# Kernel optimization log

Hardware: AMD Instinct MI355X
Metric: run time of the kernel (lower is better)

The kernel has to match this reference:

```python
import jax, jax.numpy as jnp
import numpy as np

H = 1024       # hidden_size
VOCAB = 32000  # output_size
L = 128        # max_length
B = 64         # batch


def setup_inputs() -> dict:
    key = jax.random.key(0)
    ks = jax.random.split(key, 16)
    inp = {
        "input_ids": jax.random.randint(ks[0], (1, B), 0, VOCAB),
        "hidden": jax.random.normal(ks[1], (1, B, H), jnp.float32),
        "encoder_outputs": jax.random.normal(ks[2], (L, B, H), jnp.float32),
        # parameters
        "emb": jax.random.normal(ks[3], (VOCAB, H), jnp.float32) * 0.02,
        "attn_W": jax.random.normal(ks[4], (H, 2 * H), jnp.float32) * 0.02,
        "attn_b": jnp.zeros((H,), jnp.float32),
        "v": jax.random.uniform(ks[5], (H,), jnp.float32),
        "w_ih": jax.random.normal(ks[6], (3 * H, 2 * H), jnp.float32) * 0.02,
        "w_hh": jax.random.normal(ks[7], (3 * H, H), jnp.float32) * 0.02,
        "b_ih": jnp.zeros((3 * H,), jnp.float32),
        "b_hh": jnp.zeros((3 * H,), jnp.float32),
        "out_W": jax.random.normal(ks[8], (VOCAB, 3 * H), jnp.float32) * 0.02,
        "out_b": jnp.zeros((VOCAB,), jnp.float32),
    }
    return inp


def reference(input_ids, hidden, encoder_outputs, emb, attn_W, attn_b, v,
              w_ih, w_hh, b_ih, b_hh, out_W, out_b):
    # Dropout in eval mode (identity).
    embedded = emb[input_ids]                      # [1, B, H]
    eo = jnp.transpose(encoder_outputs, (1, 0, 2))  # [B, L, H]
    h0 = hidden[0]                                  # [B, H]

    # Additive (Bahdanau) attention score
    h_rep = jnp.broadcast_to(h0[:, None, :], (eo.shape[0], eo.shape[1], h0.shape[-1]))
    cat = jnp.concatenate([eo, h_rep], axis=-1)     # [B, L, 2H]
    energy = jnp.tanh(jnp.einsum('blk,hk->blh', cat, attn_W) + attn_b)  # [B, L, H]
    scores = jnp.einsum('blh,h->bl', energy, v)     # [B, L]
    attention = jax.nn.softmax(scores, axis=-1)     # [B, L]
    weighted = jnp.einsum('bl,blh->bh', attention, eo)  # [B, H]

    # GRU cell (single layer, single timestep), PyTorch gate order r,z,n
    x = jnp.concatenate([embedded[0], weighted], axis=-1)  # [B, 2H]
    gx = x @ w_ih.T + b_ih                                  # [B, 3H]
    gh = h0 @ w_hh.T + b_hh                                 # [B, 3H]
    xr, xz, xn = jnp.split(gx, 3, axis=-1)
    hr, hz, hn = jnp.split(gh, 3, axis=-1)
    r = jax.nn.sigmoid(xr + hr)
    z = jax.nn.sigmoid(xz + hz)
    n = jnp.tanh(xn + r * hn)
    h_new = (1.0 - z) * n + z * h0                          # [B, H]

    out_cat = jnp.concatenate([h_new, weighted, embedded[0]], axis=-1)  # [B, 3H]
    output = out_cat @ out_W.T + out_b                      # [B, VOCAB]
    return output, h_new[None], attention[:, None, :]
```

## Files before the change

### kernel.cpp

```cpp
#include <hip/hip_runtime.h>
#include <math.h>

#define Hdim 1024
#define VOC 32000
#define LSEQ 128
#define BSZ 64

typedef __attribute__((ext_vector_type(8))) short bf16x8;
typedef __attribute__((ext_vector_type(4))) float f32x4;

__device__ __forceinline__ float fast_tanhf(float x) {
    return 1.0f - 2.0f / (__expf(2.0f * x) + 1.0f);
}
__device__ __forceinline__ float sigmoidf(float x) {
    return 1.0f / (1.0f + __expf(-x));
}
__device__ __forceinline__ short f2bf(float f) {
    unsigned u = __float_as_uint(f);
    unsigned r = (u + 0x7fffu + ((u >> 16) & 1u)) >> 16;
    return (short)r;
}

__device__ __forceinline__ void stage16(const float* __restrict__ src, short* dst) {
    f32x4 v0 = *(const f32x4*)(src);
    f32x4 v1 = *(const f32x4*)(src + 4);
    f32x4 v2 = *(const f32x4*)(src + 8);
    f32x4 v3 = *(const f32x4*)(src + 12);
    bf16x8 p0, p1;
    p0[0] = f2bf(v0[0]); p0[1] = f2bf(v0[1]); p0[2] = f2bf(v0[2]); p0[3] = f2bf(v0[3]);
    p0[4] = f2bf(v1[0]); p0[5] = f2bf(v1[1]); p0[6] = f2bf(v1[2]); p0[7] = f2bf(v1[3]);
    p1[0] = f2bf(v2[0]); p1[1] = f2bf(v2[1]); p1[2] = f2bf(v2[2]); p1[3] = f2bf(v2[3]);
    p1[4] = f2bf(v3[0]); p1[5] = f2bf(v3[1]); p1[6] = f2bf(v3[2]); p1[7] = f2bf(v3[3]);
    *(bf16x8*)(dst) = p0;
    *(bf16x8*)(dst + 8) = p1;
}

__global__ __launch_bounds__(256) void convert_bf16(
    const float* __restrict__ enc, const float* __restrict__ attnW,
    const float* __restrict__ hidden,
    short* __restrict__ enc_bf, short* __restrict__ attnW_bf,
    short* __restrict__ hidden_bf)
{
    const int NG_ENC = (LSEQ * BSZ * Hdim) / 8;
    const int NG_AW  = (Hdim * 2 * Hdim) / 8;
    const int NG_H   = (BSZ * Hdim) / 8;
    const int total = NG_ENC + NG_AW + NG_H;
    for (int g = blockIdx.x * 256 + threadIdx.x; g < total; g += gridDim.x * 256) {
        const float* src; short* dst; int idx;
        if (g < NG_ENC)              { src = enc;    dst = enc_bf;    idx = g; }
        else if (g < NG_ENC + NG_AW) { src = attnW;  dst = attnW_bf;  idx = g - NG_ENC; }
        else                         { src = hidden; dst = hidden_bf; idx = g - NG_ENC - NG_AW; }
        f32x4 a = *(const f32x4*)(src + (size_t)idx * 8);
        f32x4 b = *(const f32x4*)(src + (size_t)idx * 8 + 4);
        bf16x8 p;
        p[0] = f2bf(a[0]); p[1] = f2bf(a[1]); p[2] = f2bf(a[2]); p[3] = f2bf(a[3]);
        p[4] = f2bf(b[0]); p[5] = f2bf(b[1]); p[6] = f2bf(b[2]); p[7] = f2bf(b[3]);
        *(bf16x8*)(dst + (size_t)idx * 8) = p;
    }
}

__global__ __launch_bounds__(256) void ugemm(
    const short* __restrict__ A,
    const short* __restrict__ B,
    float* __restrict__ C)
{
    __shared__ short As[64 * 72];
    __shared__ short Bs[128 * 72];

    const int t = threadIdx.x;
    const int lane = t & 63, wave = t >> 6;
    const int lr = lane & 15, kh = lane >> 4;
    const int n0 = blockIdx.x * 128;
    const int kstart = blockIdx.y * 256;
    float* Cp = C + (size_t)blockIdx.y * (BSZ * Hdim);

    const int ar = t >> 2, ac = (t & 3) * 16;
    const int br = t >> 1, bc = (t & 1) * 32;

    f32x4 acc[4][2] = {};

    for (int k0 = 0; k0 < 256; k0 += 64) {
        const int kg = kstart + k0;
        {
            const short* s = A + (size_t)ar * Hdim + kg + ac;
            *(bf16x8*)(As + ar * 72 + ac)     = *(const bf16x8*)(s);
            *(bf16x8*)(As + ar * 72 + ac + 8) = *(const bf16x8*)(s + 8);
        }
        {
            const short* s = B + (size_t)(n0 + br) * (2 * Hdim) + kg + bc;
            short* d = Bs + br * 72 + bc;
            *(bf16x8*)(d)      = *(const bf16x8*)(s);
            *(bf16x8*)(d + 8)  = *(const bf16x8*)(s + 8);
            *(bf16x8*)(d + 16) = *(const bf16x8*)(s + 16);
            *(bf16x8*)(d + 24) = *(const bf16x8*)(s + 24);
        }
        __syncthreads();
#pragma unroll
        for (int kk = 0; kk < 64; kk += 32) {
            bf16x8 af[4], bfr[2];
#pragma unroll
            for (int mi = 0; mi < 4; ++mi)
                af[mi] = *(const bf16x8*)(As + (mi * 16 + lr) * 72 + kk + kh * 8);
#pragma unroll
            for (int ni = 0; ni < 2; ++ni)
                bfr[ni] = *(const bf16x8*)(Bs + (wave * 32 + ni * 16 + lr) * 72 + kk + kh * 8);
#pragma unroll
            for (int mi = 0; mi < 4; ++mi)
#pragma unroll
                for (int ni = 0; ni < 2; ++ni)
                    acc[mi][ni] = __builtin_amdgcn_mfma_f32_16x16x32_bf16(
                        af[mi], bfr[ni], acc[mi][ni], 0, 0, 0);
        }
        __syncthreads();
    }

#pragma unroll
    for (int mi = 0; mi < 4; ++mi)
#pragma unroll
        for (int ni = 0; ni < 2; ++ni) {
            const int col = n0 + wave * 32 + ni * 16 + lr;
#pragma unroll
            for (int r = 0; r < 4; ++r) {
                const int row = mi * 16 + kh * 4 + r;
                Cp[(size_t)row * Hdim + col] = acc[mi][ni][r];
            }
        }
}

__global__ __launch_bounds__(512) void attn_scores_mfma(
    const short* __restrict__ enc_bf,
    const short* __restrict__ W1_bf,
    const float* __restrict__ u4,
    const float* __restrict__ attnb,
    const float* __restrict__ vvec,
    float* __restrict__ scores_part)
{
    __shared__ short As[128 * 72];
    __shared__ short Bs[128 * 72];
    __shared__ float red[8][64];
    __shared__ float u_lds[64 * 128];

    const int t = threadIdx.x;
    const int lane = t & 63, wave = t >> 6;
    const int wr = wave >> 2, wc = wave & 3;
    const int lr = lane & 15, kh = lane >> 4;
    const int m0 = blockIdx.x * 128;
    const int n0 = blockIdx.y * 128;

    const int srow = t >> 2, scol = (t & 3) * 16;

    for (int i = t; i < 64 * 128; i += 512) {
        const int b = i >> 7, hl = i & 127;
        const size_t g = (size_t)b * Hdim + n0 + hl;
        u_lds[i] = u4[g] + u4[65536 + g] + u4[2 * 65536 + g] + u4[3 * 65536 + g]
                 + attnb[n0 + hl];
    }

    f32x4 acc[4][2] = {};

    for (int kg = 0; kg < Hdim; kg += 64) {
        {
            const short* s = enc_bf + (size_t)(m0 + srow) * Hdim + kg + scol;
            *(bf16x8*)(As + srow * 72 + scol)     = *(const bf16x8*)(s);
            *(bf16x8*)(As + srow * 72 + scol + 8) = *(const bf16x8*)(s + 8);
        }
        {
            const short* s = W1_bf + (size_t)(n0 + srow) * (2 * Hdim) + kg + scol;
            *(bf16x8*)(Bs + srow * 72 + scol)     = *(const bf16x8*)(s);
            *(bf16x8*)(Bs + srow * 72 + scol + 8) = *(const bf16x8*)(s + 8);
        }
        __syncthreads();
#pragma unroll
        for (int kk = 0; kk < 64; kk += 32) {
            bf16x8 af[4], bfr[2];
#pragma unroll
            for (int mi = 0; mi < 4; ++mi)
                af[mi] = *(const bf16x8*)(As + (wr * 64 + mi * 16 + lr) * 72 + kk + kh * 8);
#pragma unroll
            for (int ni = 0; ni < 2; ++ni)
                bfr[ni] = *(const bf16x8*)(Bs + (wc * 32 + ni * 16 + lr) * 72 + kk + kh * 8);
#pragma unroll
            for (int mi = 0; mi < 4; ++mi)
#pragma unroll
                for (int ni = 0; ni < 2; ++ni)
                    acc[mi][ni] = __builtin_amdgcn_mfma_f32_16x16x32_bf16(
                        af[mi], bfr[ni], acc[mi][ni], 0, 0, 0);
        }
        __syncthreads();
    }

    float sv[16];
#pragma unroll
    for (int mi = 0; mi < 4; ++mi)
#pragma unroll
        for (int r = 0; r < 4; ++r) {
            const int lrow = mi * 16 + kh * 4 + r;
            const int b = lrow;
            float s = 0.0f;
#pragma unroll
            for (int ni = 0; ni < 2; ++ni) {
                const int hl = wc * 32 + ni * 16 + lr;
                const float e = fast_tanhf(acc[mi][ni][r] + u_lds[b * 128 + hl]);
                s += e * vvec[n0 + hl];
            }
            sv[mi * 4 + r] = s;
        }
#pragma unroll
    for (int i = 0; i < 16; ++i) {
#pragma unroll
        for (int d = 1; d < 16; d <<= 1)
            sv[i] += __shfl_xor(sv[i], d, 64);
    }
    if (lr == 0) {
#pragma unroll
        for (int mi = 0; mi < 4; ++mi)
#pragma unroll
            for (int r = 0; r < 4; ++r)
                red[wave][mi * 16 + kh * 4 + r] = sv[mi * 4 + r];
    }
    __syncthreads();
    if (t < 128) {
        const int wrr = t >> 6, lrow = t & 63;
        scores_part[(size_t)blockIdx.y * (LSEQ * BSZ) + m0 + t] =
            red[wrr * 4 + 0][lrow] + red[wrr * 4 + 1][lrow] +
            red[wrr * 4 + 2][lrow] + red[wrr * 4 + 3][lrow];
    }
}

__global__ __launch_bounds__(256) void softmax_weighted(
    const float* __restrict__ sp,
    const short* __restrict__ enc_bf,
    const int* __restrict__ ids,
    const float* __restrict__ emb,
    float* __restrict__ attn_out,
    short* __restrict__ x_bf,
    short* __restrict__ oc_bf)
{
    const int b = blockIdx.x, t = threadIdx.x;
    __shared__ float aw[LSEQ];
    __shared__ float red[128];

    {
        const int id = ids[b];
#pragma unroll
        for (int i = 0; i < 4; ++i) {
            const int h = t * 4 + i;
            const short e = f2bf(emb[(size_t)id * Hdim + h]);
            x_bf[(size_t)b * 2048 + h] = e;
            oc_bf[(size_t)b * 3072 + 2048 + h] = e;
        }
    }

    float s = 0.0f;
    if (t < 128) {
#pragma unroll
        for (int g = 0; g < 8; ++g) s += sp[g * (LSEQ * BSZ) + t * 64 + b];
        red[t] = s;
    }
    __syncthreads();
    for (int off = 64; off > 0; off >>= 1) {
        if (t < off) red[t] = fmaxf(red[t], red[t + off]);
        __syncthreads();
    }
    const float mx = red[0];
    __syncthreads();
    float e = 0.0f;
    if (t < 128) { e = __expf(s - mx); red[t] = e; }
    __syncthreads();
    for (int off = 64; off > 0; off >>= 1) {
        if (t < off) red[t] += red[t + off];
        __syncthreads();
    }
    const float inv = 1.0f / red[0];
    if (t < 128) {
        const float p = e * inv;
        aw[t] = p;
        attn_out[(size_t)b * LSEQ + t] = p;
    }
    __syncthreads();

#pragma unroll
    for (int c = 0; c < 2; ++c) {
        const int h = c * 512 + t * 2;
        float a0 = 0.0f, a1 = 0.0f;
        for (int l = 0; l < LSEQ; ++l) {
            const unsigned w = *(const unsigned*)(enc_bf + ((size_t)l * BSZ + b) * Hdim + h);
            const float p = aw[l];
            a0 = fmaf(p, __uint_as_float(w << 16), a0);
            a1 = fmaf(p, __uint_as_float(w & 0xffff0000u), a1);
        }
        const unsigned packed = (unsigned)(unsigned short)f2bf(a0)
                              | ((unsigned)(unsigned short)f2bf(a1) << 16);
        *(unsigned*)(x_bf + (size_t)b * 2048 + 1024 + h) = packed;
        *(unsigned*)(oc_bf + (size_t)b * 3072 + 1024 + h) = packed;
    }
}

__global__ __launch_bounds__(256) void gxgh_gemm(
    const short* __restrict__ x_bf, const float* __restrict__ w_ih,
    const short* __restrict__ hidden_bf, const float* __restrict__ w_hh,
    float* __restrict__ gx4, float* __restrict__ gh4)
{
    __shared__ short As[64 * 72];
    __shared__ short Bs[128 * 72];

    const int t = threadIdx.x;
    const int lane = t & 63, wave = t >> 6;
    const int lr = lane & 15, kh = lane >> 4;

    const short* A; const float* B; float* C; int lda, klen, n0;
    if (blockIdx.x < 24) {
        A = x_bf; B = w_ih; C = gx4; lda = 2048; klen = 512; n0 = blockIdx.x * 128;
    } else {
        A = hidden_bf; B = w_hh; C = gh4; lda = 1024; klen = 256; n0 = (blockIdx.x - 24) * 128;
    }
    const int kstart = blockIdx.y * klen;
    float* Cp = C + (size_t)blockIdx.y * (BSZ * 3 * Hdim);

    const int ar = t >> 2, ac = (t & 3) * 16;
    const int br = t >> 1, bc = (t & 1) * 32;

    f32x4 acc[4][2] = {};

    for (int k0 = 0; k0 < klen; k0 += 64) {
        const int kg = kstart + k0;
        {
            const short* s = A + (size_t)ar * lda + kg + ac;
            *(bf16x8*)(As + ar * 72 + ac)     = *(const bf16x8*)(s);
            *(bf16x8*)(As + ar * 72 + ac + 8) = *(const bf16x8*)(s + 8);
        }
        {
            const float* s = B + (size_t)(n0 + br) * lda + kg + bc;
            stage16(s,      Bs + br * 72 + bc);
            stage16(s + 16, Bs + br * 72 + bc + 16);
        }
        __syncthreads();
#pragma unroll
        for (int kk = 0; kk < 64; kk += 32) {
            bf16x8 af[4], bfr[2];
#pragma unroll
            for (int mi = 0; mi < 4; ++mi)
                af[mi] = *(const bf16x8*)(As + (mi * 16 + lr) * 72 + kk + kh * 8);
#pragma unroll
            for (int ni = 0; ni < 2; ++ni)
                bfr[ni] = *(const bf16x8*)(Bs + (wave * 32 + ni * 16 + lr) * 72 + kk + kh * 8);
#pragma unroll
            for (int mi = 0; mi < 4; ++mi)
#pragma unroll
                for (int ni = 0; ni < 2; ++ni)
                    acc[mi][ni] = __builtin_amdgcn_mfma_f32_16x16x32_bf16(
                        af[mi], bfr[ni], acc[mi][ni], 0, 0, 0);
        }
        __syncthreads();
    }

#pragma unroll
    for (int mi = 0; mi < 4; ++mi)
#pragma unroll
        for (int ni = 0; ni < 2; ++ni) {
            const int col = n0 + wave * 32 + ni * 16 + lr;
#pragma unroll
            for (int r = 0; r < 4; ++r) {
                const int row = mi * 16 + kh * 4 + r;
                Cp[(size_t)row * (3 * Hdim) + col] = acc[mi][ni][r];
            }
        }
}

__global__ __launch_bounds__(256) void gru_kernel(
    const float* __restrict__ gx4, const float* __restrict__ gh4,
    const float* __restrict__ b_ih, const float* __restrict__ b_hh,
    const float* __restrict__ h0,
    float* __restrict__ hnew_out, short* __restrict__ oc_bf)
{
    const int idx = blockIdx.x * 256 + threadIdx.x;
    const int b = idx >> 10, h = idx & 1023;
    const size_t g3 = (size_t)b * (3 * Hdim);
    const size_t P = (size_t)BSZ * 3 * Hdim;
    float xr = b_ih[h], xz = b_ih[Hdim + h], xn = b_ih[2 * Hdim + h];
    float hr = b_hh[h], hz = b_hh[Hdim + h], hn = b_hh[2 * Hdim + h];
#pragma unroll
    for (int s = 0; s < 4; ++s) {
        xr += gx4[s * P + g3 + h];
        xz += gx4[s * P + g3 + Hdim + h];
        xn += gx4[s * P + g3 + 2 * Hdim + h];
        hr += gh4[s * P + g3 + h];
        hz += gh4[s * P + g3 + Hdim + h];
        hn += gh4[s * P + g3 + 2 * Hdim + h];
    }
    const float r = sigmoidf(xr + hr);
    const float z = sigmoidf(xz + hz);
    const float n = fast_tanhf(xn + r * hn);
    const float hv = (1.0f - z) * n + z * h0[(size_t)b * Hdim + h];
    hnew_out[(size_t)b * Hdim + h] = hv;
    oc_bf[g3 + h] = f2bf(hv);
}

__global__ __launch_bounds__(256) void outproj_direct(
    const short* __restrict__ A,
    const float* __restrict__ B,
    const float* __restrict__ bias,
    float* __restrict__ logits)
{
    __shared__ short As[64 * 72];
    __shared__ short Bs[64 * 72];

    const int t = threadIdx.x;
    const int lane = t & 63, wave = t >> 6;
    const int lr = lane & 15, kh = lane >> 4;
    const int n0 = blockIdx.x * 64;
    const int sr = t >> 2, sc = (t & 3) * 16;

    f32x4 acc[4] = {};

    for (int kg = 0; kg < 3072; kg += 64) {
        {
            const short* s = A + (size_t)sr * 3072 + kg + sc;
            *(bf16x8*)(As + sr * 72 + sc)     = *(const bf16x8*)(s);
            *(bf16x8*)(As + sr * 72 + sc + 8) = *(const bf16x8*)(s + 8);
        }
        stage16(B + (size_t)(n0 + sr) * 3072 + kg + sc, Bs + sr * 72 + sc);
        __syncthreads();
#pragma unroll
        for (int kk = 0; kk < 64; kk += 32) {
            bf16x8 af[4], bfr;
#pragma unroll
            for (int mi = 0; mi < 4; ++mi)
                af[mi] = *(const bf16x8*)(As + (mi * 16 + lr) * 72 + kk + kh * 8);
            bfr = *(const bf16x8*)(Bs + (wave * 16 + lr) * 72 + kk + kh * 8);
#pragma unroll
            for (int mi = 0; mi < 4; ++mi)
                acc[mi] = __builtin_amdgcn_mfma_f32_16x16x32_bf16(af[mi], bfr, acc[mi], 0, 0, 0);
        }
        __syncthreads();
    }

    const int col = n0 + wave * 16 + lr;
    const float bb = bias[col];
#pragma unroll
    for (int mi = 0; mi < 4; ++mi)
#pragma unroll
        for (int r = 0; r < 4; ++r) {
            const int row = mi * 16 + kh * 4 + r;
            logits[(size_t)row * VOC + col] = acc[mi][r] + bb;
        }
}

extern "C" void kernel_launch(void* const* d_in, const int* in_sizes, int n_in,
                              void* d_out, int out_size, void* d_ws, size_t ws_size,
                              hipStream_t stream)
{
    const int*   ids    = (const int*)d_in[0];
    const float* hidden = (const float*)d_in[1];
    const float* enc    = (const float*)d_in[2];
    const float* emb    = (const float*)d_in[3];
    const float* attnW  = (const float*)d_in[4];
    const float* attnb  = (const float*)d_in[5];
    const float* vvec   = (const float*)d_in[6];
    const float* w_ih   = (const float*)d_in[7];
    const float* w_hh   = (const float*)d_in[8];
    const float* b_ih   = (const float*)d_in[9];
    const float* b_hh   = (const float*)d_in[10];
    const float* out_W  = (const float*)d_in[11];
    const float* out_b  = (const float*)d_in[12];

    float* out        = (float*)d_out;
    float* out_logits = out;
    float* out_hnew   = out + (size_t)BSZ * VOC;
    float* out_attn   = out_hnew + (size_t)BSZ * Hdim;

    float* ws = (float*)d_ws;
    short* enc_bf    = (short*)ws;
    short* attnW_bf  = (short*)(ws + 4194304);
    short* hidden_bf = (short*)(ws + 5242880);
    float* ws_u4  = ws + 5275648;
    float* ws_sp  = ws_u4 + 262144;
    short* x_bf   = (short*)(ws_sp + 65536);
    short* oc_bf  = (short*)(ws_sp + 131072);
    float* ws_gx4 = ws_sp + 229376;
    float* ws_gh4 = ws_gx4 + 786432;

    convert_bf16<<<dim3(1024), 256, 0, stream>>>(
        enc, attnW, hidden, enc_bf, attnW_bf, hidden_bf);

    ugemm<<<dim3(Hdim / 128, 4), 256, 0, stream>>>(
        hidden_bf, attnW_bf + Hdim, ws_u4);

    attn_scores_mfma<<<dim3(LSEQ / 2, 8), 512, 0, stream>>>(
        enc_bf, attnW_bf, ws_u4, attnb, vvec, ws_sp);

    softmax_weighted<<<dim3(BSZ), 256, 0, stream>>>(
        ws_sp, enc_bf, ids, emb, out_attn, x_bf, oc_bf);

    gxgh_gemm<<<dim3(48, 4), 256, 0, stream>>>(
        x_bf, w_ih, hidden_bf, w_hh, ws_gx4, ws_gh4);

    gru_kernel<<<dim3(BSZ * Hdim / 256), 256, 0, stream>>>(
        ws_gx4, ws_gh4, b_ih, b_hh, hidden, out_hnew, oc_bf);

    outproj_direct<<<dim3(VOC / 64), 256, 0, stream>>>(
        oc_bf, out_W, out_b, out_logits);
}
```

Baseline: 190.0 us.

## Stream weights directly into MFMA registers, drop LDS staging; split softmax-weighted over hidden

Replaces the LDS-staged GEMMs for the GRU gates and output projection with a shared streaming body. Each lane loads its fp32 weight row slice, converts it to bf16 in registers and feeds MFMA directly, with no shared memory or barriers. The activation A operand is read from global memory/L2 by each wave. The gate GEMM now uses 64-column tiles, doubling its grid. The softmax/weighted-sum kernel is split across 4 hidden-dimension groups with 128 threads each for more parallelism, and uses vectorised embedding loads. The trade is that A reads repeat across waves instead of being shared, in exchange for removing sync and LDS traffic in these memory-bound weight-streaming GEMMs.

```diff
diff --git a/kernel.cpp b/kernel.cpp
--- a/kernel.cpp
+++ b/kernel.cpp
@@ -19,20 +19,6 @@
     unsigned u = __float_as_uint(f);
     unsigned r = (u + 0x7fffu + ((u >> 16) & 1u)) >> 16;
     return (short)r;
-}
-
-__device__ __forceinline__ void stage16(const float* __restrict__ src, short* dst) {
-    f32x4 v0 = *(const f32x4*)(src);
-    f32x4 v1 = *(const f32x4*)(src + 4);
-    f32x4 v2 = *(const f32x4*)(src + 8);
-    f32x4 v3 = *(const f32x4*)(src + 12);
-    bf16x8 p0, p1;
-    p0[0] = f2bf(v0[0]); p0[1] = f2bf(v0[1]); p0[2] = f2bf(v0[2]); p0[3] = f2bf(v0[3]);
-    p0[4] = f2bf(v1[0]); p0[5] = f2bf(v1[1]); p0[6] = f2bf(v1[2]); p0[7] = f2bf(v1[3]);
-    p1[0] = f2bf(v2[0]); p1[1] = f2bf(v2[1]); p1[2] = f2bf(v2[2]); p1[3] = f2bf(v2[3]);
-    p1[4] = f2bf(v3[0]); p1[5] = f2bf(v3[1]); p1[6] = f2bf(v3[2]); p1[7] = f2bf(v3[3]);
-    *(bf16x8*)(dst) = p0;
-    *(bf16x8*)(dst + 8) = p1;
 }
 
 __global__ __launch_bounds__(256) void convert_bf16(
@@ -227,7 +213,7 @@
     }
 }
 
-__global__ __launch_bounds__(256) void softmax_weighted(
+__global__ __launch_bounds__(128) void softmax_weighted(
     const float* __restrict__ sp,
     const short* __restrict__ enc_bf,
     const int* __restrict__ ids,
@@ -236,27 +222,26 @@
     short* __restrict__ x_bf,
     short* __restrict__ oc_bf)
 {
-    const int b = blockIdx.x, t = threadIdx.x;
+    const int b = blockIdx.x, hg = blockIdx.y, t = threadIdx.x;
     __shared__ float aw[LSEQ];
-    __shared__ float red[128];
-
-    {
+    __shared__ float red[LSEQ];
+
+    if (hg == 0) {
         const int id = ids[b];
-#pragma unroll
-        for (int i = 0; i < 4; ++i) {
-            const int h = t * 4 + i;
-            const short e = f2bf(emb[(size_t)id * Hdim + h]);
-            x_bf[(size_t)b * 2048 + h] = e;
-            oc_bf[(size_t)b * 3072 + 2048 + h] = e;
-        }
+        const int h = t * 8;
+        f32x4 e0 = *(const f32x4*)(emb + (size_t)id * Hdim + h);
+        f32x4 e1 = *(const f32x4*)(emb + (size_t)id * Hdim + h + 4);
+        bf16x8 p;
+        p[0] = f2bf(e0[0]); p[1] = f2bf(e0[1]); p[2] = f2bf(e0[2]); p[3] = f2bf(e0[3]);
+        p[4] = f2bf(e1[0]); p[5] = f2bf(e1[1]); p[6] = f2bf(e1[2]); p[7] = f2bf(e1[3]);
+        *(bf16x8*)(x_bf + (size_t)b * 2048 + h) = p;
+        *(bf16x8*)(oc_bf + (size_t)b * 3072 + 2048 + h) = p;
     }
 
     float s = 0.0f;
-    if (t < 128) {
-#pragma unroll
-        for (int g = 0; g < 8; ++g) s += sp[g * (LSEQ * BSZ) + t * 64 + b];
-        red[t] = s;
-    }
+#pragma unroll
+    for (int g = 0; g < 8; ++g) s += sp[g * (LSEQ * BSZ) + t * 64 + b];
+    red[t] = s;
     __syncthreads();
     for (int off = 64; off > 0; off >>= 1) {
         if (t < off) red[t] = fmaxf(red[t], red[t + off]);
@@ -264,107 +249,94 @@
     }
     const float mx = red[0];
     __syncthreads();
-    float e = 0.0f;
-    if (t < 128) { e = __expf(s - mx); red[t] = e; }
+    const float e = __expf(s - mx);
+    red[t] = e;
     __syncthreads();
     for (int off = 64; off > 0; off >>= 1) {
         if (t < off) red[t] += red[t + off];
         __syncthreads();
     }
-    const float inv = 1.0f / red[0];
-    if (t < 128) {
-        const float p = e * inv;
-        aw[t] = p;
-        attn_out[(size_t)b * LSEQ + t] = p;
-    }
+    const float p = e / red[0];
+    aw[t] = p;
+    if (hg == 0) attn_out[(size_t)b * LSEQ + t] = p;
     __syncthreads();
 
-#pragma unroll
-    for (int c = 0; c < 2; ++c) {
-        const int h = c * 512 + t * 2;
-        float a0 = 0.0f, a1 = 0.0f;
-        for (int l = 0; l < LSEQ; ++l) {
-            const unsigned w = *(const unsigned*)(enc_bf + ((size_t)l * BSZ + b) * Hdim + h);
-            const float p = aw[l];
-            a0 = fmaf(p, __uint_as_float(w << 16), a0);
-            a1 = fmaf(p, __uint_as_float(w & 0xffff0000u), a1);
-        }
-        const unsigned packed = (unsigned)(unsigned short)f2bf(a0)
-                              | ((unsigned)(unsigned short)f2bf(a1) << 16);
-        *(unsigned*)(x_bf + (size_t)b * 2048 + 1024 + h) = packed;
-        *(unsigned*)(oc_bf + (size_t)b * 3072 + 1024 + h) = packed;
-    }
-}
-
-__global__ __launch_bounds__(256) void gxgh_gemm(
+    const int h = hg * 256 + t * 2;
+    float a0 = 0.0f, a1 = 0.0f;
+#pragma unroll 8
+    for (int l = 0; l < LSEQ; ++l) {
+        const unsigned w = *(const unsigned*)(enc_bf + ((size_t)l * BSZ + b) * Hdim + h);
+        const float pw = aw[l];
+        a0 = fmaf(pw, __uint_as_float(w << 16), a0);
+        a1 = fmaf(pw, __uint_as_float(w & 0xffff0000u), a1);
+    }
+    const unsigned packed = (unsigned)(unsigned short)f2bf(a0)
+                          | ((unsigned)(unsigned short)f2bf(a1) << 16);
+    *(unsigned*)(x_bf + (size_t)b * 2048 + 1024 + h) = packed;
+    *(unsigned*)(oc_bf + (size_t)b * 3072 + 1024 + h) = packed;
+}
+
+__device__ __forceinline__ void stream_body(
+    const short* __restrict__ A, int lda,
+    const float* __restrict__ B, int ldb,
+    const float* __restrict__ bias,
+    float* __restrict__ C, int ldc,
+    int n0, int kstart, int klen)
+{
+    const int t = threadIdx.x;
+    const int lane = t & 63, wave = t >> 6;
+    const int lr = lane & 15, kh = lane >> 4;
+
+    const float* Brow = B + (size_t)(n0 + wave * 16 + lr) * ldb + kh * 8 + kstart;
+    const short* Ab   = A + (size_t)lr * lda + kh * 8 + kstart;
+
+    f32x4 acc[4] = {};
+
+#pragma unroll 4
+    for (int kg = 0; kg < klen; kg += 32) {
+        f32x4 b0 = *(const f32x4*)(Brow + kg);
+        f32x4 b1 = *(const f32x4*)(Brow + kg + 4);
+        bf16x8 bfr;
+        bfr[0] = f2bf(b0[0]); bfr[1] = f2bf(b0[1]); bfr[2] = f2bf(b0[2]); bfr[3] = f2bf(b0[3]);
+        bfr[4] = f2bf(b1[0]); bfr[5] = f2bf(b1[1]); bfr[6] = f2bf(b1[2]); bfr[7] = f2bf(b1[3]);
+#pragma unroll
+        for (int mi = 0; mi < 4; ++mi) {
+            bf16x8 af = *(const bf16x8*)(Ab + (size_t)mi * 16 * lda + kg);
+            acc[mi] = __builtin_amdgcn_mfma_f32_16x16x32_bf16(af, bfr, acc[mi], 0, 0, 0);
+        }
+    }
+
+    const int col = n0 + wave * 16 + lr;
+    const float bb = bias ? bias[col] : 0.0f;
+#pragma unroll
+    for (int mi = 0; mi < 4; ++mi)
+#pragma unroll
+        for (int r = 0; r < 4; ++r)
+            C[(size_t)(mi * 16 + kh * 4 + r) * ldc + col] = acc[mi][r] + bb;
+}
+
+__global__ __launch_bounds__(256) void outproj_stream(
+    const short* __restrict__ A, const float* __restrict__ B,
+    const float* __restrict__ bias, float* __restrict__ logits)
+{
+    stream_body(A, 3 * Hdim, B, 3 * Hdim, bias, logits, VOC,
+                blockIdx.x * 64, 0, 3 * Hdim);
+}
+
+__global__ __launch_bounds__(256) void gxgh_stream(
     const short* __restrict__ x_bf, const float* __restrict__ w_ih,
     const short* __restrict__ hidden_bf, const float* __restrict__ w_hh,
     float* __restrict__ gx4, float* __restrict__ gh4)
 {
-    __shared__ short As[64 * 72];
-    __shared__ short Bs[128 * 72];
-
-    const int t = threadIdx.x;
-    const int lane = t & 63, wave = t >> 6;
-    const int lr = lane & 15, kh = lane >> 4;
-
-    const short* A; const float* B; float* C; int lda, klen, n0;
-    if (blockIdx.x < 24) {
-        A = x_bf; B = w_ih; C = gx4; lda = 2048; klen = 512; n0 = blockIdx.x * 128;
-    } else {
-        A = hidden_bf; B = w_hh; C = gh4; lda = 1024; klen = 256; n0 = (blockIdx.x - 24) * 128;
-    }
-    const int kstart = blockIdx.y * klen;
-    float* Cp = C + (size_t)blockIdx.y * (BSZ * 3 * Hdim);
-
-    const int ar = t >> 2, ac = (t & 3) * 16;
-    const int br = t >> 1, bc = (t & 1) * 32;
-
-    f32x4 acc[4][2] = {};
-
-    for (int k0 = 0; k0 < klen; k0 += 64) {
-        const int kg = kstart + k0;
-        {
-            const short* s = A + (size_t)ar * lda + kg + ac;
-            *(bf16x8*)(As + ar * 72 + ac)     = *(const bf16x8*)(s);
-            *(bf16x8*)(As + ar * 72 + ac + 8) = *(const bf16x8*)(s + 8);
-        }
-        {
-            const float* s = B + (size_t)(n0 + br) * lda + kg + bc;
-            stage16(s,      Bs + br * 72 + bc);
-            stage16(s + 16, Bs + br * 72 + bc + 16);
-        }
-        __syncthreads();
-#pragma unroll
-        for (int kk = 0; kk < 64; kk += 32) {
-            bf16x8 af[4], bfr[2];
-#pragma unroll
-            for (int mi = 0; mi < 4; ++mi)
-                af[mi] = *(const bf16x8*)(As + (mi * 16 + lr) * 72 + kk + kh * 8);
-#pragma unroll
-            for (int ni = 0; ni < 2; ++ni)
-                bfr[ni] = *(const bf16x8*)(Bs + (wave * 32 + ni * 16 + lr) * 72 + kk + kh * 8);
-#pragma unroll
-            for (int mi = 0; mi < 4; ++mi)
-#pragma unroll
-                for (int ni = 0; ni < 2; ++ni)
-                    acc[mi][ni] = __builtin_amdgcn_mfma_f32_16x16x32_bf16(
-                        af[mi], bfr[ni], acc[mi][ni], 0, 0, 0);
-        }
-        __syncthreads();
-    }
-
-#pragma unroll
-    for (int mi = 0; mi < 4; ++mi)
-#pragma unroll
-        for (int ni = 0; ni < 2; ++ni) {
-            const int col = n0 + wave * 32 + ni * 16 + lr;
-#pragma unroll
-            for (int r = 0; r < 4; ++r) {
-                const int row = mi * 16 + kh * 4 + r;
-                Cp[(size_t)row * (3 * Hdim) + col] = acc[mi][ni][r];
-            }
-        }
+    const size_t P = (size_t)BSZ * 3 * Hdim;
+    if (blockIdx.x < 48)
+        stream_body(x_bf, 2 * Hdim, w_ih, 2 * Hdim, nullptr,
+                    gx4 + blockIdx.y * P, 3 * Hdim,
+                    blockIdx.x * 64, blockIdx.y * 512, 512);
+    else
+        stream_body(hidden_bf, Hdim, w_hh, Hdim, nullptr,
+                    gh4 + blockIdx.y * P, 3 * Hdim,
+                    (blockIdx.x - 48) * 64, blockIdx.y * 256, 256);
 }
 
 __global__ __launch_bounds__(256) void gru_kernel(
@@ -394,56 +366,6 @@
     const float hv = (1.0f - z) * n + z * h0[(size_t)b * Hdim + h];
     hnew_out[(size_t)b * Hdim + h] = hv;
     oc_bf[g3 + h] = f2bf(hv);
-}
-
-__global__ __launch_bounds__(256) void outproj_direct(
-    const short* __restrict__ A,
-    const float* __restrict__ B,
-    const float* __restrict__ bias,
-    float* __restrict__ logits)
-{
-    __shared__ short As[64 * 72];
-    __shared__ short Bs[64 * 72];
-
-    const int t = threadIdx.x;
-    const int lane = t & 63, wave = t >> 6;
-    const int lr = lane & 15, kh = lane >> 4;
-    const int n0 = blockIdx.x * 64;
-    const int sr = t >> 2, sc = (t & 3) * 16;
-
-    f32x4 acc[4] = {};
-
-    for (int kg = 0; kg < 3072; kg += 64) {
-        {
-            const short* s = A + (size_t)sr * 3072 + kg + sc;
-            *(bf16x8*)(As + sr * 72 + sc)     = *(const bf16x8*)(s);
-            *(bf16x8*)(As + sr * 72 + sc + 8) = *(const bf16x8*)(s + 8);
-        }
-        stage16(B + (size_t)(n0 + sr) * 3072 + kg + sc, Bs + sr * 72 + sc);
-        __syncthreads();
-#pragma unroll
-        for (int kk = 0; kk < 64; kk += 32) {
-            bf16x8 af[4], bfr;
-#pragma unroll
-            for (int mi = 0; mi < 4; ++mi)
-                af[mi] = *(const bf16x8*)(As + (mi * 16 + lr) * 72 + kk + kh * 8);
-            bfr = *(const bf16x8*)(Bs + (wave * 16 + lr) * 72 + kk + kh * 8);
-#pragma unroll
-            for (int mi = 0; mi < 4; ++mi)
-                acc[mi] = __builtin_amdgcn_mfma_f32_16x16x32_bf16(af[mi], bfr, acc[mi], 0, 0, 0);
-        }
-        __syncthreads();
-    }
-
-    const int col = n0 + wave * 16 + lr;
-    const float bb = bias[col];
-#pragma unroll
-    for (int mi = 0; mi < 4; ++mi)
-#pragma unroll
-        for (int r = 0; r < 4; ++r) {
-            const int row = mi * 16 + kh * 4 + r;
-            logits[(size_t)row * VOC + col] = acc[mi][r] + bb;
-        }
 }
 
 extern "C" void kernel_launch(void* const* d_in, const int* in_sizes, int n_in,
@@ -489,15 +411,15 @@
     attn_scores_mfma<<<dim3(LSEQ / 2, 8), 512, 0, stream>>>(
         enc_bf, attnW_bf, ws_u4, attnb, vvec, ws_sp);
 
-    softmax_weighted<<<dim3(BSZ), 256, 0, stream>>>(
+    softmax_weighted<<<dim3(BSZ, 4), 128, 0, stream>>>(
         ws_sp, enc_bf, ids, emb, out_attn, x_bf, oc_bf);
 
-    gxgh_gemm<<<dim3(48, 4), 256, 0, stream>>>(
+    gxgh_stream<<<dim3(96, 4), 256, 0, stream>>>(
         x_bf, w_ih, hidden_bf, w_hh, ws_gx4, ws_gh4);
 
     gru_kernel<<<dim3(BSZ * Hdim / 256), 256, 0, stream>>>(
         ws_gx4, ws_gh4, b_ih, b_hh, hidden, out_hnew, oc_bf);
 
-    outproj_direct<<<dim3(VOC / 64), 256, 0, stream>>>(
+    outproj_stream<<<dim3(VOC / 64), 256, 0, stream>>>(
         oc_bf, out_W, out_b, out_logits);
 }
```

Measured after the change: 232.0 us. 1.22x slower.
